# Kernel optimization log

Measured on AMD Instinct MI355X. Metric: run time of the kernel, lower is better.

The kernel has to match this reference:

```python
import jax, jax.numpy as jnp
import numpy as np

NUM_CLASSES = 80
D_IMG = 2048
D_WORD = 300
D_MID = 1024
B = 8
CONV = 14


def setup_inputs() -> dict:
    key = jax.random.key(0)
    ks = jax.random.split(key, 6)
    s = lambda k, shape, sc: jax.random.normal(k, shape, dtype=jnp.float32) * sc
    return {
        "batch_size": B,
        "img_feature_map": jax.random.normal(ks[0], (B, D_IMG, CONV, CONV), dtype=jnp.float32),
        "word_features": jax.random.normal(ks[1], (NUM_CLASSES, D_WORD), dtype=jnp.float32),
        "W1": s(ks[2], (D_MID, D_IMG), 0.02),
        "W2": s(ks[3], (D_MID, D_WORD), 0.02),
        "W3": s(ks[4], (D_MID, D_MID), 0.02),
        "b3": jnp.zeros((D_MID,), jnp.float32),
        "Wa": s(ks[5], (1, D_MID), 0.02),
        "ba": jnp.zeros((1,), jnp.float32),
    }


def reference(batch_size, img_feature_map, word_features, W1, W2, W3, b3, Wa, ba):
    # img_feature_map: [B, D_img, H, W] -> [B, H, W, D_img] (matches torch double transpose)
    Bn, D, H, W = img_feature_map.shape
    fmap = jnp.transpose(img_feature_map, (0, 2, 3, 1))                 # [B,H,W,D]
    f_wh = jnp.einsum('bhwd,md->bhwm', fmap, W1)                        # fc_1: [B,H,W,M]
    f_wd = word_features @ W2.T                                         # fc_2: [C,M]
    # broadcast multiply (no explicit repeat) + tanh
    t = jnp.tanh(f_wh[:, :, :, None, :] * f_wd)                         # [B,H,W,C,M]
    lb = jnp.einsum('bhwcm,nm->bhwcn', t, W3) + b3                      # fc_3: [B,H,W,C,M]
    coef = jnp.einsum('bhwcm,m->bhwc', lb, Wa[0]) + ba[0]               # fc_a: [B,H,W,C]
    # softmax over spatial positions per (batch, class)
    C = coef.shape[-1]
    coef = jax.nn.softmax(coef.reshape(Bn, H * W, C), axis=1).reshape(Bn, H, W, C)
    # softmax-weighted spatial pooling -> [B, C, D]
    return jnp.einsum('bhwc,bhwd->bcd', coef, fmap)
```

## Files before the change

### kernel.cpp

```cpp
#include <hip/hip_runtime.h>
#include <hip/hip_bf16.h>
#include <stdint.h>

#define NB 8
#define DIMG 2048
#define HWN 196
#define PN 1568
#define DMID 1024
#define NC 80
#define DWORD 300
#define PART 8

typedef short bf16x8 __attribute__((ext_vector_type(8)));
typedef float f32x4 __attribute__((ext_vector_type(4)));

__device__ __forceinline__ unsigned short f2bf(float x) {
  union { float f; unsigned u; } c; c.f = x;
  unsigned r = c.u + 0x7FFFu + ((c.u >> 16) & 1u);
  return (unsigned short)(r >> 16);
}

__global__ void k_tc(const float* __restrict__ img, unsigned short* __restrict__ fmapH,
                     const float* __restrict__ W1, unsigned short* __restrict__ W1h) {
  __shared__ float tile[64][33];
  int bx = blockIdx.x;
  int tx = threadIdx.x, ty = threadIdx.y;
  if (bx < 1792) {
    int d0 = (bx & 31) * 64;
    int rem = bx >> 5;
    int h0 = (rem % 7) * 32, b = rem / 7;
    const float* src = img + (size_t)b * DIMG * HWN;
#pragma unroll
    for (int i = 0; i < 64; i += 8) {
      int hw = h0 + tx;
      tile[ty + i][tx] = (hw < HWN) ? src[(size_t)(d0 + ty + i) * HWN + hw] : 0.f;
    }
    __syncthreads();
#pragma unroll
    for (int i = 0; i < 32; i += 8) {
      int hw = h0 + ty + i;
      if (hw < HWN) {
        int d = tx * 2;
        unsigned short lo = f2bf(tile[d][ty + i]);
        unsigned short hi = f2bf(tile[d + 1][ty + i]);
        unsigned v = (unsigned)lo | ((unsigned)hi << 16);
        *(unsigned*)&fmapH[(size_t)(b * HWN + hw) * DIMG + d0 + d] = v;
      }
    }
  } else {
    int tid = ty * 32 + tx;
    int i = ((bx - 1792) * 256 + tid) * 4;
    f32x4 v = *(const f32x4*)(W1 + i);
    ushort4 s;
    s.x = f2bf(v[0]); s.y = f2bf(v[1]); s.z = f2bf(v[2]); s.w = f2bf(v[3]);
    *(ushort4*)(W1h + i) = s;
  }
}

#define GLDS(g, l) \
  __builtin_amdgcn_global_load_lds((const __attribute__((address_space(1))) void*)(g), \
                                   (__attribute__((address_space(3))) void*)(l), 16, 0, 0)

__global__ __launch_bounds__(256) void k_gw(const unsigned short* __restrict__ A,
                                            const unsigned short* __restrict__ Bw,
                                            float* __restrict__ C,
                                            const float* __restrict__ word,
                                            const float* __restrict__ W2,
                                            float* __restrict__ fwd,
                                            const float* __restrict__ Wa,
                                            const float* __restrict__ W3,
                                            float* __restrict__ partial) {
  __shared__ __align__(16) char smem[49152];
  int bz = blockIdx.x;
  int t = threadIdx.x;
  if (bz < 800) {
    unsigned short* As = (unsigned short*)smem;
    unsigned short* Bs = As + 3 * 4096;
    int m0 = (bz % 25) * 64;
    int n0 = ((bz / 25) & 15) * 64;
    int koff = (bz / 400) * 1024;
    int w = t >> 6, l = t & 63;
    int wr = w >> 1, wc = w & 1;
    f32x4 zero = {0.f, 0.f, 0.f, 0.f};
    f32x4 acc00 = zero, acc01 = zero, acc10 = zero, acc11 = zero;

    int r0 = t >> 3, c0 = t & 7;
    int r1 = r0 + 32;
    const unsigned short* ga0 = A + (size_t)(m0 + r0) * 2048 + koff + ((c0 ^ (r0 & 7)) << 3);
    const unsigned short* ga1 = A + (size_t)(m0 + r1) * 2048 + koff + ((c0 ^ (r1 & 7)) << 3);
    const unsigned short* gb0 = Bw + (size_t)(n0 + r0) * 2048 + koff + ((c0 ^ (r0 & 7)) << 3);
    const unsigned short* gb1 = Bw + (size_t)(n0 + r1) * 2048 + koff + ((c0 ^ (r1 & 7)) << 3);

    int ra = wr * 32 + (l & 15);
    int rb = wc * 32 + (l & 15);
    int cc = l >> 4;
    int a_k0 = ra * 64 + (((cc) ^ (ra & 7)) << 3);
    int a_k1 = ra * 64 + (((cc + 4) ^ (ra & 7)) << 3);
    int b_k0 = rb * 64 + (((cc) ^ (rb & 7)) << 3);
    int b_k1 = rb * 64 + (((cc + 4) ^ (rb & 7)) << 3);

#define STAGE(bi, kk) do { \
    GLDS(ga0 + (kk), As + (bi) * 4096 + t * 8); \
    GLDS(ga1 + (kk), As + (bi) * 4096 + t * 8 + 2048); \
    GLDS(gb0 + (kk), Bs + (bi) * 4096 + t * 8); \
    GLDS(gb1 + (kk), Bs + (bi) * 4096 + t * 8 + 2048); \
  } while (0)
#define COMPUTE(bi) do { \
    const unsigned short* ap = As + (bi) * 4096; \
    const unsigned short* bp = Bs + (bi) * 4096; \
    bf16x8 A0 = *(const bf16x8*)(ap + a_k0); \
    bf16x8 A1 = *(const bf16x8*)(ap + a_k0 + 1024); \
    bf16x8 B0 = *(const bf16x8*)(bp + b_k0); \
    bf16x8 B1 = *(const bf16x8*)(bp + b_k0 + 1024); \
    acc00 = __builtin_amdgcn_mfma_f32_16x16x32_bf16(A0, B0, acc00, 0, 0, 0); \
    acc01 = __builtin_amdgcn_mfma_f32_16x16x32_bf16(A0, B1, acc01, 0, 0, 0); \
    acc10 = __builtin_amdgcn_mfma_f32_16x16x32_bf16(A1, B0, acc10, 0, 0, 0); \
    acc11 = __builtin_amdgcn_mfma_f32_16x16x32_bf16(A1, B1, acc11, 0, 0, 0); \
    bf16x8 A2 = *(const bf16x8*)(ap + a_k1); \
    bf16x8 A3 = *(const bf16x8*)(ap + a_k1 + 1024); \
    bf16x8 B2 = *(const bf16x8*)(bp + b_k1); \
    bf16x8 B3 = *(const bf16x8*)(bp + b_k1 + 1024); \
    acc00 = __builtin_amdgcn_mfma_f32_16x16x32_bf16(A2, B2, acc00, 0, 0, 0); \
    acc01 = __builtin_amdgcn_mfma_f32_16x16x32_bf16(A2, B3, acc01, 0, 0, 0); \
    acc10 = __builtin_amdgcn_mfma_f32_16x16x32_bf16(A3, B2, acc10, 0, 0, 0); \
    acc11 = __builtin_amdgcn_mfma_f32_16x16x32_bf16(A3, B3, acc11, 0, 0, 0); \
  } while (0)

    STAGE(0, 0);
    STAGE(1, 64);
    asm volatile("s_waitcnt vmcnt(4)" ::: "memory");
    __builtin_amdgcn_s_barrier();
    __builtin_amdgcn_sched_barrier(0);
    for (int kt = 0; kt < 16; ++kt) {
      int cur = kt % 3;
      if (kt < 14) STAGE((kt + 2) % 3, (kt + 2) * 64);
      COMPUTE(cur);
      if (kt < 14) {
        asm volatile("s_waitcnt vmcnt(4)" ::: "memory");
        __builtin_amdgcn_s_barrier();
        __builtin_amdgcn_sched_barrier(0);
      } else if (kt == 14) {
        asm volatile("s_waitcnt vmcnt(0)" ::: "memory");
        __builtin_amdgcn_s_barrier();
        __builtin_amdgcn_sched_barrier(0);
      }
    }
    float* Cz = C + (size_t)(bz / 400) * (1600 * DMID);
    int cr = (l >> 4) << 2, ccn = l & 15;
#pragma unroll
    for (int q = 0; q < 4; ++q) {
      Cz[(size_t)(m0 + wr * 32 + cr + q) * DMID + n0 + wc * 32 + ccn] = acc00[q];
      Cz[(size_t)(m0 + wr * 32 + cr + q) * DMID + n0 + wc * 32 + 16 + ccn] = acc01[q];
      Cz[(size_t)(m0 + wr * 32 + 16 + cr + q) * DMID + n0 + wc * 32 + ccn] = acc10[q];
      Cz[(size_t)(m0 + wr * 32 + 16 + cr + q) * DMID + n0 + wc * 32 + 16 + ccn] = acc11[q];
    }
#undef STAGE
#undef COMPUTE
  } else if (bz < 1120) {
    float* w2s = (float*)smem;
    float* wds = w2s + 16 * 300;
    int idx = bz - 800;
    int m0 = (idx & 63) * 16, c0 = (idx >> 6) * 16;
    const float SC = 2.8853900817779268f;
    for (int u = t; u < 16 * 75; u += 256) {
      int r = u / 75, q = u - r * 75;
      *(f32x4*)&w2s[r * 300 + q * 4] = *(const f32x4*)(W2 + (size_t)(m0 + r) * DWORD + q * 4);
      f32x4 v = *(const f32x4*)(word + (size_t)(c0 + r) * DWORD + q * 4);
      *(f32x4*)&wds[r * 300 + q * 4] = v * SC;
    }
    __syncthreads();
    int ci = t >> 4, mi = t & 15;
    f32x4 av = {0.f, 0.f, 0.f, 0.f};
    const float* wr_ = &wds[ci * 300];
    const float* w2r = &w2s[mi * 300];
    for (int q = 0; q < 75; ++q) {
      f32x4 wv = *(const f32x4*)&wr_[q * 4];
      f32x4 bv = *(const f32x4*)&w2r[q * 4];
#pragma unroll
      for (int u = 0; u < 4; ++u) av[u] = fmaf(wv[u], bv[u], av[u]);
    }
    fwd[(size_t)(c0 + ci) * DMID + m0 + mi] = av[0] + av[1] + av[2] + av[3];
  } else {
    int idx = bz - 1120;
    int m = (idx & 3) * 256 + t;
    int n0 = (idx >> 2) * 64;
    float acc = 0.f;
    for (int n = n0; n < n0 + 64; ++n) acc = fmaf(Wa[n], W3[(size_t)n * DMID + m], acc);
    partial[(size_t)(idx >> 2) * DMID + m] = acc;
  }
}

#define MC 64
__global__ __launch_bounds__(256) void k_coef(const float* __restrict__ fwhp,
                                              const float* __restrict__ fwd,
                                              const float* __restrict__ partial,
                                              float* __restrict__ coefp) {
  __shared__ __align__(16) float al[32][68];
  __shared__ __align__(16) float bl[16][68];
  __shared__ __align__(16) float wl[MC];
  int p0 = blockIdx.x * 32, c0 = blockIdx.y * 16, mz = blockIdx.z;
  int t = threadIdx.x;
  int pi = t >> 4, ci = t & 15;
  float acc[2] = {0.f, 0.f};
  const float* fwh0 = fwhp;
  const float* fwh1 = fwhp + (size_t)1600 * DMID;

  for (int mc = 0; mc < 2; ++mc) {
    int mbase = mz * 128 + mc * MC;
    __syncthreads();
    {
      int sra = t >> 3, sca = (t & 7) << 3;
      const float* gA0 = fwh0 + (size_t)(p0 + sra) * DMID + mbase + sca;
      const float* gA1 = fwh1 + (size_t)(p0 + sra) * DMID + mbase + sca;
#pragma unroll
      for (int q = 0; q < 2; ++q) {
        f32x4 v = *(const f32x4*)&gA0[q * 4];
        f32x4 u = *(const f32x4*)&gA1[q * 4];
        *(f32x4*)&al[sra][sca + q * 4] = v + u;
      }
      int srb = t >> 4, scb = (t & 15) << 2;
      *(f32x4*)&bl[srb][scb] = *(const f32x4*)(fwd + (size_t)(c0 + srb) * DMID + mbase + scb);
      if (t < MC) {
        float v = 0.f;
#pragma unroll
        for (int s = 0; s < 16; ++s) v += partial[(size_t)s * DMID + mbase + t];
        wl[t] = -2.f * v;
      }
    }
    __syncthreads();
    for (int mm = 0; mm < MC; mm += 4) {
      f32x4 wv = *(const f32x4*)&wl[mm];
      f32x4 bv = *(const f32x4*)&bl[ci][mm];
      f32x4 av0 = *(const f32x4*)&al[pi][mm];
      f32x4 av1 = *(const f32x4*)&al[pi + 16][mm];
#pragma unroll
      for (int u = 0; u < 4; ++u) {
        float w = wv[u], b = bv[u];
        float e0 = __builtin_amdgcn_exp2f(av0[u] * b);
        float e1 = __builtin_amdgcn_exp2f(av1[u] * b);
        acc[0] = fmaf(w, __builtin_amdgcn_rcpf(1.f + e0), acc[0]);
        acc[1] = fmaf(w, __builtin_amdgcn_rcpf(1.f + e1), acc[1]);
      }
    }
  }
  float* cp = coefp + (size_t)mz * (PN * NC);
#pragma unroll
  for (int j = 0; j < 2; ++j) {
    int p = p0 + pi + 16 * j;
    if (p < PN) cp[(size_t)p * NC + c0 + ci] = acc[j];
  }
}

__global__ __launch_bounds__(256) void k_pool(const float* __restrict__ coefp,
                                              const float* __restrict__ img,
                                              float* __restrict__ out) {
  __shared__ __align__(16) float wt[HWN][16];
  __shared__ float red[16][16];
  __shared__ float mxs[16], inv[16];
  int dc = blockIdx.x * 256, cg = blockIdx.y * 16, b = blockIdx.z;
  int t = threadIdx.x;
  for (int i = t; i < HWN * 4; i += 256) {
    int hw = i >> 2, j4 = (i & 3) << 2;
    size_t o = (size_t)(b * HWN + hw) * NC + cg + j4;
    f32x4 s = {0.f, 0.f, 0.f, 0.f};
#pragma unroll
    for (int z = 0; z < PART; ++z) s += *(const f32x4*)&coefp[o + (size_t)z * (PN * NC)];
    *(f32x4*)&wt[hw][j4] = s;
  }
  __syncthreads();
  int j = t & 15, g = t >> 4;
  float pm = -1e30f;
  for (int hw = g; hw < HWN; hw += 16) pm = fmaxf(pm, wt[hw][j]);
  red[g][j] = pm;
  __syncthreads();
  if (t < 16) {
    float m = red[0][t];
#pragma unroll
    for (int g2 = 1; g2 < 16; ++g2) m = fmaxf(m, red[g2][t]);
    mxs[t] = m;
  }
  __syncthreads();
  float mj = mxs[j], ps = 0.f;
  for (int hw = g; hw < HWN; hw += 16) {
    float e = __builtin_amdgcn_exp2f((wt[hw][j] - mj) * 1.4426950408889634f);
    wt[hw][j] = e;
    ps += e;
  }
  red[g][j] = ps;
  __syncthreads();
  if (t < 16) {
    float s = 0.f;
#pragma unroll
    for (int g2 = 0; g2 < 16; ++g2) s += red[g2][t];
    inv[t] = 1.f / s;
  }
  __syncthreads();
  float acc[16];
#pragma unroll
  for (int q = 0; q < 16; ++q) acc[q] = 0.f;
  const float* fpd = img + ((size_t)b * DIMG + dc + t) * HWN;
  for (int hw = 0; hw < HWN; ++hw) {
    float v = fpd[hw];
#pragma unroll
    for (int q = 0; q < 16; ++q) acc[q] = fmaf(wt[hw][q], v, acc[q]);
  }
#pragma unroll
  for (int q = 0; q < 16; ++q)
    out[((size_t)b * NC + cg + q) * DIMG + dc + t] = acc[q] * inv[q];
}

extern "C" void kernel_launch(void* const* d_in, const int* in_sizes, int n_in,
                              void* d_out, int out_size, void* d_ws, size_t ws_size,
                              hipStream_t stream) {
  const float* img  = (const float*)d_in[1];
  const float* word = (const float*)d_in[2];
  const float* W1   = (const float*)d_in[3];
  const float* W2   = (const float*)d_in[4];
  const float* W3   = (const float*)d_in[5];
  const float* Wa   = (const float*)d_in[7];
  float* out = (float*)d_out;
  char* ws = (char*)d_ws;

  unsigned short* fmapH   = (unsigned short*)(ws + 0);
  unsigned short* W1h     = (unsigned short*)(ws + 6553600);
  float*          fwhp    = (float*)(ws + 10747904);
  float*          fwd     = (float*)(ws + 23855104);
  float*          partial = (float*)(ws + 24248320);
  float*          coefp   = (float*)(ws + 24313856);

  hipLaunchKernelGGL(k_tc, dim3(3840), dim3(32, 8), 0, stream, img, fmapH, W1, W1h);
  hipLaunchKernelGGL(k_gw, dim3(1184), dim3(256), 0, stream,
                     fmapH, W1h, fwhp, word, W2, fwd, Wa, W3, partial);
  hipLaunchKernelGGL(k_coef, dim3(49, 5, 8), dim3(256), 0, stream, fwhp, fwd, partial, coefp);
  hipLaunchKernelGGL(k_pool, dim3(8, 5, 8), dim3(256), 0, stream, coefp, img, out);
  (void)in_sizes; (void)n_in; (void)out_size; (void)ws_size;
}
```

Measured before the change: 103.6 us.

## Retile fc_1 GEMM to 128x128 tiles with 4-way split-K

The bf16 MFMA GEMM moves from 64x64 tiles with 2-way split-K and a triple-buffered pipeline to 128x128 tiles (4x4 MFMA accumulators per wave) with 4-way split-K and a single buffered LDS stage that syncs twice per iteration. k_coef now sums four partial outputs instead of two, and the workspace offsets grow to hold them. The aim is more data reuse per tile. The cost is losing the load/compute overlap and the LDS swizzle (possible bank conflicts), plus doubled partial-result traffic through global memory. Rows past 1600 are masked because the M tile no longer divides evenly.

```diff
diff --git a/kernel.cpp b/kernel.cpp
--- a/kernel.cpp
+++ b/kernel.cpp
@@ -10,6 +10,7 @@
 #define NC 80
 #define DWORD 300
 #define PART 8
+#define KSPLIT 4
 
 typedef short bf16x8 __attribute__((ext_vector_type(8)));
 typedef float f32x4 __attribute__((ext_vector_type(4)));
@@ -70,96 +71,70 @@
                                             const float* __restrict__ Wa,
                                             const float* __restrict__ W3,
                                             float* __restrict__ partial) {
-  __shared__ __align__(16) char smem[49152];
+  __shared__ __align__(16) char smem[38400];
   int bz = blockIdx.x;
   int t = threadIdx.x;
-  if (bz < 800) {
+  if (bz < 416) {
     unsigned short* As = (unsigned short*)smem;
-    unsigned short* Bs = As + 3 * 4096;
-    int m0 = (bz % 25) * 64;
-    int n0 = ((bz / 25) & 15) * 64;
-    int koff = (bz / 400) * 1024;
+    unsigned short* Bs = As + 4096;
+    int m0 = (bz % 13) * 128;
+    int n0 = ((bz / 13) & 7) * 128;
+    int koff = (bz / 104) * 512;
     int w = t >> 6, l = t & 63;
     int wr = w >> 1, wc = w & 1;
     f32x4 zero = {0.f, 0.f, 0.f, 0.f};
-    f32x4 acc00 = zero, acc01 = zero, acc10 = zero, acc11 = zero;
-
-    int r0 = t >> 3, c0 = t & 7;
-    int r1 = r0 + 32;
-    const unsigned short* ga0 = A + (size_t)(m0 + r0) * 2048 + koff + ((c0 ^ (r0 & 7)) << 3);
-    const unsigned short* ga1 = A + (size_t)(m0 + r1) * 2048 + koff + ((c0 ^ (r1 & 7)) << 3);
-    const unsigned short* gb0 = Bw + (size_t)(n0 + r0) * 2048 + koff + ((c0 ^ (r0 & 7)) << 3);
-    const unsigned short* gb1 = Bw + (size_t)(n0 + r1) * 2048 + koff + ((c0 ^ (r1 & 7)) << 3);
-
-    int ra = wr * 32 + (l & 15);
-    int rb = wc * 32 + (l & 15);
-    int cc = l >> 4;
-    int a_k0 = ra * 64 + (((cc) ^ (ra & 7)) << 3);
-    int a_k1 = ra * 64 + (((cc + 4) ^ (ra & 7)) << 3);
-    int b_k0 = rb * 64 + (((cc) ^ (rb & 7)) << 3);
-    int b_k1 = rb * 64 + (((cc + 4) ^ (rb & 7)) << 3);
-
-#define STAGE(bi, kk) do { \
-    GLDS(ga0 + (kk), As + (bi) * 4096 + t * 8); \
-    GLDS(ga1 + (kk), As + (bi) * 4096 + t * 8 + 2048); \
-    GLDS(gb0 + (kk), Bs + (bi) * 4096 + t * 8); \
-    GLDS(gb1 + (kk), Bs + (bi) * 4096 + t * 8 + 2048); \
-  } while (0)
-#define COMPUTE(bi) do { \
-    const unsigned short* ap = As + (bi) * 4096; \
-    const unsigned short* bp = Bs + (bi) * 4096; \
-    bf16x8 A0 = *(const bf16x8*)(ap + a_k0); \
-    bf16x8 A1 = *(const bf16x8*)(ap + a_k0 + 1024); \
-    bf16x8 B0 = *(const bf16x8*)(bp + b_k0); \
-    bf16x8 B1 = *(const bf16x8*)(bp + b_k0 + 1024); \
-    acc00 = __builtin_amdgcn_mfma_f32_16x16x32_bf16(A0, B0, acc00, 0, 0, 0); \
-    acc01 = __builtin_amdgcn_mfma_f32_16x16x32_bf16(A0, B1, acc01, 0, 0, 0); \
-    acc10 = __builtin_amdgcn_mfma_f32_16x16x32_bf16(A1, B0, acc10, 0, 0, 0); \
-    acc11 = __builtin_amdgcn_mfma_f32_16x16x32_bf16(A1, B1, acc11, 0, 0, 0); \
-    bf16x8 A2 = *(const bf16x8*)(ap + a_k1); \
-    bf16x8 A3 = *(const bf16x8*)(ap + a_k1 + 1024); \
-    bf16x8 B2 = *(const bf16x8*)(bp + b_k1); \
-    bf16x8 B3 = *(const bf16x8*)(bp + b_k1 + 1024); \
-    acc00 = __builtin_amdgcn_mfma_f32_16x16x32_bf16(A2, B2, acc00, 0, 0, 0); \
-    acc01 = __builtin_amdgcn_mfma_f32_16x16x32_bf16(A2, B3, acc01, 0, 0, 0); \
-    acc10 = __builtin_amdgcn_mfma_f32_16x16x32_bf16(A3, B2, acc10, 0, 0, 0); \
-    acc11 = __builtin_amdgcn_mfma_f32_16x16x32_bf16(A3, B3, acc11, 0, 0, 0); \
-  } while (0)
-
-    STAGE(0, 0);
-    STAGE(1, 64);
-    asm volatile("s_waitcnt vmcnt(4)" ::: "memory");
-    __builtin_amdgcn_s_barrier();
-    __builtin_amdgcn_sched_barrier(0);
-    for (int kt = 0; kt < 16; ++kt) {
-      int cur = kt % 3;
-      if (kt < 14) STAGE((kt + 2) % 3, (kt + 2) * 64);
-      COMPUTE(cur);
-      if (kt < 14) {
-        asm volatile("s_waitcnt vmcnt(4)" ::: "memory");
-        __builtin_amdgcn_s_barrier();
-        __builtin_amdgcn_sched_barrier(0);
-      } else if (kt == 14) {
-        asm volatile("s_waitcnt vmcnt(0)" ::: "memory");
-        __builtin_amdgcn_s_barrier();
-        __builtin_amdgcn_sched_barrier(0);
-      }
-    }
-    float* Cz = C + (size_t)(bz / 400) * (1600 * DMID);
-    int cr = (l >> 4) << 2, ccn = l & 15;
-#pragma unroll
-    for (int q = 0; q < 4; ++q) {
-      Cz[(size_t)(m0 + wr * 32 + cr + q) * DMID + n0 + wc * 32 + ccn] = acc00[q];
-      Cz[(size_t)(m0 + wr * 32 + cr + q) * DMID + n0 + wc * 32 + 16 + ccn] = acc01[q];
-      Cz[(size_t)(m0 + wr * 32 + 16 + cr + q) * DMID + n0 + wc * 32 + ccn] = acc10[q];
-      Cz[(size_t)(m0 + wr * 32 + 16 + cr + q) * DMID + n0 + wc * 32 + 16 + ccn] = acc11[q];
-    }
-#undef STAGE
-#undef COMPUTE
-  } else if (bz < 1120) {
+    f32x4 acc[4][4];
+#pragma unroll
+    for (int i = 0; i < 4; ++i)
+#pragma unroll
+      for (int j = 0; j < 4; ++j) acc[i][j] = zero;
+
+    int sr = t >> 2, sk = (t & 3) << 3;
+    const unsigned short* ga0 = A + (size_t)(m0 + sr) * 2048 + koff + sk;
+    const unsigned short* ga1 = A + (size_t)(m0 + 64 + sr) * 2048 + koff + sk;
+    const unsigned short* gb0 = Bw + (size_t)(n0 + sr) * 2048 + koff + sk;
+    const unsigned short* gb1 = Bw + (size_t)(n0 + 64 + sr) * 2048 + koff + sk;
+
+    int fr = l & 15, ko = (l >> 4) << 3;
+
+    for (int kk = 0; kk < 512; kk += 32) {
+      __syncthreads();
+      GLDS(ga0 + kk, As + t * 8);
+      GLDS(ga1 + kk, As + t * 8 + 2048);
+      GLDS(gb0 + kk, Bs + t * 8);
+      GLDS(gb1 + kk, Bs + t * 8 + 2048);
+      __syncthreads();
+      bf16x8 a[4], b[4];
+#pragma unroll
+      for (int i = 0; i < 4; ++i)
+        a[i] = *(const bf16x8*)&As[(wr * 64 + i * 16 + fr) * 32 + ko];
+#pragma unroll
+      for (int j = 0; j < 4; ++j)
+        b[j] = *(const bf16x8*)&Bs[(wc * 64 + j * 16 + fr) * 32 + ko];
+#pragma unroll
+      for (int i = 0; i < 4; ++i)
+#pragma unroll
+        for (int j = 0; j < 4; ++j)
+          acc[i][j] = __builtin_amdgcn_mfma_f32_16x16x32_bf16(a[i], b[j], acc[i][j], 0, 0, 0);
+    }
+    float* Cz = C + (size_t)(bz / 104) * (1600 * DMID);
+    int cr = (l >> 4) << 2, cc2 = l & 15;
+#pragma unroll
+    for (int i = 0; i < 4; ++i) {
+#pragma unroll
+      for (int q = 0; q < 4; ++q) {
+        int row = m0 + wr * 64 + i * 16 + cr + q;
+        if (row < 1600) {
+#pragma unroll
+          for (int j = 0; j < 4; ++j)
+            Cz[(size_t)row * DMID + n0 + wc * 64 + j * 16 + cc2] = acc[i][j][q];
+        }
+      }
+    }
+  } else if (bz < 736) {
     float* w2s = (float*)smem;
     float* wds = w2s + 16 * 300;
-    int idx = bz - 800;
+    int idx = bz - 416;
     int m0 = (idx & 63) * 16, c0 = (idx >> 6) * 16;
     const float SC = 2.8853900817779268f;
     for (int u = t; u < 16 * 75; u += 256) {
@@ -181,10 +156,11 @@
     }
     fwd[(size_t)(c0 + ci) * DMID + m0 + mi] = av[0] + av[1] + av[2] + av[3];
   } else {
-    int idx = bz - 1120;
+    int idx = bz - 736;
     int m = (idx & 3) * 256 + t;
     int n0 = (idx >> 2) * 64;
     float acc = 0.f;
+#pragma unroll 4
     for (int n = n0; n < n0 + 64; ++n) acc = fmaf(Wa[n], W3[(size_t)n * DMID + m], acc);
     partial[(size_t)(idx >> 2) * DMID + m] = acc;
   }
@@ -202,21 +178,21 @@
   int t = threadIdx.x;
   int pi = t >> 4, ci = t & 15;
   float acc[2] = {0.f, 0.f};
-  const float* fwh0 = fwhp;
-  const float* fwh1 = fwhp + (size_t)1600 * DMID;
+  const size_t FS = (size_t)1600 * DMID;
 
   for (int mc = 0; mc < 2; ++mc) {
     int mbase = mz * 128 + mc * MC;
     __syncthreads();
     {
       int sra = t >> 3, sca = (t & 7) << 3;
-      const float* gA0 = fwh0 + (size_t)(p0 + sra) * DMID + mbase + sca;
-      const float* gA1 = fwh1 + (size_t)(p0 + sra) * DMID + mbase + sca;
+      const float* gA = fwhp + (size_t)(p0 + sra) * DMID + mbase + sca;
 #pragma unroll
       for (int q = 0; q < 2; ++q) {
-        f32x4 v = *(const f32x4*)&gA0[q * 4];
-        f32x4 u = *(const f32x4*)&gA1[q * 4];
-        *(f32x4*)&al[sra][sca + q * 4] = v + u;
+        f32x4 v = *(const f32x4*)&gA[q * 4];
+        v += *(const f32x4*)&gA[FS + q * 4];
+        v += *(const f32x4*)&gA[2 * FS + q * 4];
+        v += *(const f32x4*)&gA[3 * FS + q * 4];
+        *(f32x4*)&al[sra][sca + q * 4] = v;
       }
       int srb = t >> 4, scb = (t & 15) << 2;
       *(f32x4*)&bl[srb][scb] = *(const f32x4*)(fwd + (size_t)(c0 + srb) * DMID + mbase + scb);
@@ -322,14 +298,14 @@
   char* ws = (char*)d_ws;
 
   unsigned short* fmapH   = (unsigned short*)(ws + 0);
-  unsigned short* W1h     = (unsigned short*)(ws + 6553600);
-  float*          fwhp    = (float*)(ws + 10747904);
-  float*          fwd     = (float*)(ws + 23855104);
-  float*          partial = (float*)(ws + 24248320);
-  float*          coefp   = (float*)(ws + 24313856);
+  unsigned short* W1h     = (unsigned short*)(ws + 6815744);
+  float*          fwhp    = (float*)(ws + 11010048);
+  float*          fwd     = (float*)(ws + 37224448);
+  float*          partial = (float*)(ws + 37617664);
+  float*          coefp   = (float*)(ws + 37683200);
 
   hipLaunchKernelGGL(k_tc, dim3(3840), dim3(32, 8), 0, stream, img, fmapH, W1, W1h);
-  hipLaunchKernelGGL(k_gw, dim3(1184), dim3(256), 0, stream,
+  hipLaunchKernelGGL(k_gw, dim3(800), dim3(256), 0, stream,
                      fmapH, W1h, fwhp, word, W2, fwd, Wa, W3, partial);
   hipLaunchKernelGGL(k_coef, dim3(49, 5, 8), dim3(256), 0, stream, fwhp, fwd, partial, coefp);
   hipLaunchKernelGGL(k_pool, dim3(8, 5, 8), dim3(256), 0, stream, coefp, img, out);
```

After: 100.2 us. -3.4%, faster.
